# Performance work log

Hardware: AMD Instinct MI355X
Metric: run time of the kernel (lower is better)

## Reference

```python
import jax, jax.numpy as jnp
import numpy as np

B, L, D, H = 2, 2048, 1024, 16
HD = D // H
HID = 4 * D
EPS = 1e-5


def setup_inputs() -> dict:
    key = jax.random.key(0)
    ks = jax.random.split(key, 16)
    s = 0.02
    inp = {
        "x": jax.random.normal(ks[0], (B, L, D), jnp.float32),
        "mask": jnp.triu(jnp.ones((L, L), bool), k=1),  # True above diagonal -> masked
        "wq": jax.random.normal(ks[1], (D, D), jnp.float32) * s,
        "wk": jax.random.normal(ks[2], (D, D), jnp.float32) * s,
        "wv": jax.random.normal(ks[3], (D, D), jnp.float32) * s,
        "wo": jax.random.normal(ks[4], (D, D), jnp.float32) * s,
        "ln1_g": jnp.ones((D,), jnp.float32),
        "ln1_b": jnp.zeros((D,), jnp.float32),
        "ln2_g": jnp.ones((D,), jnp.float32),
        "ln2_b": jnp.zeros((D,), jnp.float32),
        "w1": jax.random.normal(ks[5], (HID, D), jnp.float32) * s,
        "b1": jnp.zeros((HID,), jnp.float32),
        "wg": jax.random.normal(ks[6], (HID, D), jnp.float32) * s,
        "w2": jax.random.normal(ks[7], (D, HID), jnp.float32) * s,
        "b2": jnp.zeros((D,), jnp.float32),
    }
    return inp


def _layernorm(x, g, b):
    mu = jnp.mean(x, axis=-1, keepdims=True)
    var = jnp.mean(jnp.square(x - mu), axis=-1, keepdims=True)
    return (x - mu) * jax.lax.rsqrt(var + EPS) * g + b


def _attention(h, mask, wq, wk, wv, wo):
    b, l, d = h.shape
    scale = HD ** -0.5
    # torch Linear: y = x @ W.T (W is [out, in])
    q = (h @ wq.T).reshape(b, l, H, HD)
    k = (h @ wk.T).reshape(b, l, H, HD)
    v = (h @ wv.T).reshape(b, l, H, HD)
    attn = jnp.einsum("bqhd,bkhd->bhqk", q, k) * scale
    attn = jnp.where(mask[None, None, :, :], -jnp.inf, attn)
    pos_bias = jnp.arange(l, dtype=attn.dtype) * 0.01  # additive bias along key axis
    attn = attn + pos_bias[None, None, None, :]
    attn = jax.nn.softmax(attn, axis=-1)
    out = jnp.einsum("bhqk,bkhd->bqhd", attn, v).reshape(b, l, d)
    return out @ wo.T


def _ffn(h, w1, b1, wg, w2, b2):
    return (jax.nn.silu(h @ w1.T + b1) * (h @ wg.T)) @ w2.T + b2


def reference(x, mask, wq, wk, wv, wo, ln1_g, ln1_b, ln2_g, ln2_b, w1, b1, wg, w2, b2):
    x = x + _attention(_layernorm(x, ln1_g, ln1_b), mask, wq, wk, wv, wo)
    x = x + _ffn(_layernorm(x, ln2_g, ln2_b), w1, b1, wg, w2, b2)
    return x
```

## Files before the change

### kernel.cpp

```cpp
#include <hip/hip_runtime.h>

#define ML   2048
#define MD   1024
#define MH   16
#define MHD  64
#define MB   2
#define MM   4096
#define MHID 4096

typedef unsigned short u16;
typedef short bf16x8 __attribute__((ext_vector_type(8)));
typedef float f32x4 __attribute__((ext_vector_type(4)));

__device__ __forceinline__ u16 f2bf(float f) {
    union { float f; unsigned u; } c; c.f = f;
    unsigned r = c.u + 0x7fffu + ((c.u >> 16) & 1u);
    return (u16)(r >> 16);
}
__device__ __forceinline__ float bf2f(u16 h) {
    union { unsigned u; float f; } c; c.u = ((unsigned)h) << 16;
    return c.f;
}

__device__ __forceinline__ void async_copy16(const u16* g, u16* l) {
    __builtin_amdgcn_global_load_lds(
        (const __attribute__((address_space(1))) void*)g,
        (__attribute__((address_space(3))) void*)l, 16, 0, 0);
}

struct ConvPack {
    const float* src[13];
    u16* dst[13];
    int n[13];
    int start[14];
};

__global__ __launch_bounds__(256)
void conv_all(ConvPack p)
{
    const int bx = blockIdx.x;
    int seg = 0;
    while (seg < 12 && bx >= p.start[seg + 1]) ++seg;
    const int local = bx - p.start[seg];
    const int idx = (local * 256 + threadIdx.x) * 8;
    if (idx >= p.n[seg]) return;
    const float* in = p.src[seg];
    const float4 a = *(const float4*)(in + idx);
    const float4 b = *(const float4*)(in + idx + 4);
    union { bf16x8 v; u16 s[8]; } u;
    u.s[0] = f2bf(a.x); u.s[1] = f2bf(a.y); u.s[2] = f2bf(a.z); u.s[3] = f2bf(a.w);
    u.s[4] = f2bf(b.x); u.s[5] = f2bf(b.y); u.s[6] = f2bf(b.z); u.s[7] = f2bf(b.w);
    *(bf16x8*)&p.dst[seg][idx] = u.v;
}

template<int MI, int NI>
__device__ __forceinline__ void gemm_core(
    const u16* __restrict__ A, const u16* __restrict__ Bm,
    int m0, int n0, int K, u16* As, u16* Bs, f32x4 (&acc)[MI][NI])
{
    constexpr int TM = MI * 32;
    constexpr int TN = NI * 32;
    const int tid  = threadIdx.x;
    const int wave = tid >> 6, lane = tid & 63;
    const int wm = wave & 1, wn = wave >> 1;
    const int l15 = lane & 15, quad = lane >> 4;

    const int srow = wave * 16 + (lane >> 2);
    const int scol = (lane & 3) * 8;
    const u16* Ag = A  + (size_t)(m0 + srow) * K + scol;
    const u16* Bg = Bm + (size_t)(n0 + srow) * K + scol;
    u16* Asw = As + srow * 32 + scol;
    u16* Bsw = Bs + srow * 32 + scol;

    f32x4 zero4 = {0.f, 0.f, 0.f, 0.f};
#pragma unroll
    for (int mi = 0; mi < MI; ++mi)
#pragma unroll
        for (int ni = 0; ni < NI; ++ni) acc[mi][ni] = zero4;

    for (int k0 = 0; k0 < K; k0 += 32) {
        __syncthreads();
#pragma unroll
        for (int p = 0; p < TM / 64; ++p)
            async_copy16(Ag + k0 + (size_t)p * 64 * K, Asw + p * 64 * 32);
#pragma unroll
        for (int p = 0; p < TN / 64; ++p)
            async_copy16(Bg + k0 + (size_t)p * 64 * K, Bsw + p * 64 * 32);
        __syncthreads();

        bf16x8 af[MI], bfr[NI];
#pragma unroll
        for (int mi = 0; mi < MI; ++mi)
            af[mi] = *(const bf16x8*)&As[(wm * MI * 16 + mi * 16 + l15) * 32 + quad * 8];
#pragma unroll
        for (int ni = 0; ni < NI; ++ni)
            bfr[ni] = *(const bf16x8*)&Bs[(wn * NI * 16 + ni * 16 + l15) * 32 + quad * 8];
#pragma unroll
        for (int mi = 0; mi < MI; ++mi)
#pragma unroll
            for (int ni = 0; ni < NI; ++ni)
                acc[mi][ni] = __builtin_amdgcn_mfma_f32_16x16x32_bf16(
                    af[mi], bfr[ni], acc[mi][ni], 0, 0, 0);
    }
}

__global__ __launch_bounds__(256)
void ln_kernel(const float* __restrict__ xin,
               const u16* __restrict__ g, const u16* __restrict__ bb,
               u16* __restrict__ out)
{
    const int row = blockIdx.x;
    const int tid = threadIdx.x;
    const float4 t = *(const float4*)(xin + (size_t)row * MD + tid * 4);
    float v[4] = {t.x, t.y, t.z, t.w};
    float s  = v[0] + v[1] + v[2] + v[3];
    float s2 = v[0]*v[0] + v[1]*v[1] + v[2]*v[2] + v[3]*v[3];
#pragma unroll
    for (int off = 1; off < 64; off <<= 1) {
        s  += __shfl_xor(s,  off);
        s2 += __shfl_xor(s2, off);
    }
    __shared__ float red[8];
    const int wave = tid >> 6, lane = tid & 63;
    if (lane == 0) { red[wave] = s; red[4 + wave] = s2; }
    __syncthreads();
    s  = red[0] + red[1] + red[2] + red[3];
    s2 = red[4] + red[5] + red[6] + red[7];
    const float mu  = s * (1.0f / MD);
    const float var = fmaxf(s2 * (1.0f / MD) - mu * mu, 0.0f);
    const float rs  = rsqrtf(var + 1e-5f);
    const ushort4 gv = *(const ushort4*)&g[tid * 4];
    const ushort4 bv = *(const ushort4*)&bb[tid * 4];
    ushort4 o;
    o.x = f2bf((v[0] - mu) * rs * bf2f(gv.x) + bf2f(bv.x));
    o.y = f2bf((v[1] - mu) * rs * bf2f(gv.y) + bf2f(bv.y));
    o.z = f2bf((v[2] - mu) * rs * bf2f(gv.z) + bf2f(bv.z));
    o.w = f2bf((v[3] - mu) * rs * bf2f(gv.w) + bf2f(bv.w));
    *(ushort4*)&out[(size_t)row * MD + tid * 4] = o;
}

__global__ __launch_bounds__(256, 2)
void gemm_qkv(const u16* __restrict__ ln, const u16* __restrict__ wq,
              const u16* __restrict__ wk, const u16* __restrict__ wv,
              u16* __restrict__ q, u16* __restrict__ k, u16* __restrict__ vt)
{
    __shared__ __align__(16) u16 As[128 * 32];
    __shared__ __align__(16) u16 Bs[128 * 32];
    const int z = blockIdx.z;
    const u16* Bm = (z == 0) ? wq : (z == 1) ? wk : wv;
    const int m0 = blockIdx.x * 128, n0 = blockIdx.y * 128;
    f32x4 acc[4][4];
    gemm_core<4, 4>(ln, Bm, m0, n0, MD, As, Bs, acc);

    const int tid = threadIdx.x;
    const int wave = tid >> 6, lane = tid & 63;
    const int wm = wave & 1, wn = wave >> 1, l15 = lane & 15, quad = lane >> 4;
    if (z < 2) {
        u16* out = (z == 0) ? q : k;
        const float scale = (z == 0) ? 0.125f : 1.0f;
#pragma unroll
        for (int mi = 0; mi < 4; ++mi)
#pragma unroll
            for (int ni = 0; ni < 4; ++ni)
#pragma unroll
                for (int r = 0; r < 4; ++r) {
                    const int row = m0 + wm * 64 + mi * 16 + quad * 4 + r;
                    const int col = n0 + wn * 64 + ni * 16 + l15;
                    out[(size_t)row * MD + col] = f2bf(acc[mi][ni][r] * scale);
                }
    } else {
#pragma unroll
        for (int mi = 0; mi < 4; ++mi)
#pragma unroll
            for (int ni = 0; ni < 4; ++ni) {
                const int row0 = m0 + wm * 64 + mi * 16 + quad * 4;
                const int col  = n0 + wn * 64 + ni * 16 + l15;
                const int bb = row0 >> 11, l = row0 & (ML - 1);
                const int hh = col >> 6,  hd = col & (MHD - 1);
                ushort4 pk;
                pk.x = f2bf(acc[mi][ni][0]);
                pk.y = f2bf(acc[mi][ni][1]);
                pk.z = f2bf(acc[mi][ni][2]);
                pk.w = f2bf(acc[mi][ni][3]);
                *(ushort4*)&vt[((size_t)(bb * MH + hh) * MHD + hd) * ML + l] = pk;
            }
    }
}

__global__ __launch_bounds__(256, 2)
void attn_kernel(const u16* __restrict__ Q, const u16* __restrict__ Kb,
                 const u16* __restrict__ Vt, u16* __restrict__ O)
{
    __shared__ __align__(16) u16 Ks[64 * 64];
    __shared__ __align__(16) u16 Vs[64 * 64];
    __shared__ __align__(16) u16 Pl[4][16 * 72];
    const int tid = threadIdx.x, wave = tid >> 6, lane = tid & 63;
    const int quad = lane >> 4, l15 = lane & 15;
    const int idx = blockIdx.x;
    const int qt = (ML / 64 - 1) - (idx >> 5);
    const int hb = idx & 31;
    const int h = hb & 15, b = hb >> 4;
    const int q0 = qt * 64;
    const int qrow = q0 + wave * 16;
    const float L2E = 1.44269504f;
    const float C1 = 0.01f * L2E;
    const float C2 = -32.0f * L2E;

    u16* Plw = Pl[wave];

    const size_t qoff = ((size_t)(b * ML + qrow + l15)) * MD + h * MHD + quad * 8;
    const bf16x8 aq0 = *(const bf16x8*)&Q[qoff];
    const bf16x8 aq1 = *(const bf16x8*)&Q[qoff + 32];

    const int str = tid >> 3;
    const int sj  = tid & 7;
    const int sjx = (sj ^ (str & 7)) * 8;
    const u16* Kg = Kb + (size_t)(b * ML) * MD + h * MHD;
    const u16* Vg = Vt + (size_t)((b * MH + h) * MHD) * ML;

    const int rsw0 = ((quad    ) ^ (l15 & 7)) * 8;
    const int rsw1 = ((quad + 4) ^ (l15 & 7)) * 8;

    bf16x8 onesf;
    {
        const short v = (l15 == 0) ? (short)0x3F80 : (short)0;
        onesf = (bf16x8){v, v, v, v, v, v, v, v};
    }

    f32x4 zero4 = {0.f, 0.f, 0.f, 0.f};
    f32x4 Oacc[4];
    f32x4 lsum = zero4;
#pragma unroll
    for (int i = 0; i < 4; ++i) Oacc[i] = zero4;

    for (int kt = 0; kt <= qt; ++kt) {
        const int k0 = kt * 64;

        __syncthreads();
        async_copy16(Kg + (size_t)(k0 + str) * MD + sjx,        Ks + tid * 8);
        async_copy16(Kg + (size_t)(k0 + 32 + str) * MD + sjx,   Ks + 2048 + tid * 8);
        async_copy16(Vg + (size_t)str * ML + k0 + sjx,          Vs + tid * 8);
        async_copy16(Vg + (size_t)(32 + str) * ML + k0 + sjx,   Vs + 2048 + tid * 8);
        __syncthreads();

        f32x4 s[4];
#pragma unroll
        for (int jn = 0; jn < 4; ++jn) {
            const int krow = (jn * 16 + l15) * 64;
            const bf16x8 k0f = *(const bf16x8*)&Ks[krow + rsw0];
            const bf16x8 k1f = *(const bf16x8*)&Ks[krow + rsw1];
            f32x4 z = zero4;
            z = __builtin_amdgcn_mfma_f32_16x16x32_bf16(aq0, k0f, z, 0, 0, 0);
            z = __builtin_amdgcn_mfma_f32_16x16x32_bf16(aq1, k1f, z, 0, 0, 0);
            s[jn] = z;
        }

        const bool diag = (kt == qt);
#pragma unroll
        for (int jn = 0; jn < 4; ++jn) {
            const int key = k0 + jn * 16 + l15;
            const float pbm = fmaf((float)key, C1, C2);
#pragma unroll
            for (int r = 0; r < 4; ++r) {
                float val = fmaf(s[jn][r], L2E, pbm);
                if (diag && key > qrow + quad * 4 + r) val = -30000.f;
                union { float f; unsigned u; } c;
                c.f = exp2f(val);
                Plw[(quad * 4 + r) * 72 + jn * 16 + l15] = (u16)(c.u >> 16);
            }
        }

        bf16x8 vv[4][2];
#pragma unroll
        for (int j = 0; j < 4; ++j) {
            const int vrow = (j * 16 + l15) * 64;
            vv[j][0] = *(const bf16x8*)&Vs[vrow + rsw0];
            vv[j][1] = *(const bf16x8*)&Vs[vrow + rsw1];
        }

        const bf16x8 ap0 = *(const bf16x8*)&Plw[l15 * 72 + quad * 8];
        const bf16x8 ap1 = *(const bf16x8*)&Plw[l15 * 72 + 32 + quad * 8];
#pragma unroll
        for (int j = 0; j < 4; ++j) {
            Oacc[j] = __builtin_amdgcn_mfma_f32_16x16x32_bf16(ap0, vv[j][0], Oacc[j], 0, 0, 0);
            Oacc[j] = __builtin_amdgcn_mfma_f32_16x16x32_bf16(ap1, vv[j][1], Oacc[j], 0, 0, 0);
        }
        lsum = __builtin_amdgcn_mfma_f32_16x16x32_bf16(ap0, onesf, lsum, 0, 0, 0);
        lsum = __builtin_amdgcn_mfma_f32_16x16x32_bf16(ap1, onesf, lsum, 0, 0, 0);
    }

#pragma unroll
    for (int r = 0; r < 4; ++r) {
        const float l = __shfl(lsum[r], lane & 48);
        const float inv = 1.0f / l;
        const int row = qrow + quad * 4 + r;
#pragma unroll
        for (int j = 0; j < 4; ++j) {
            const int col = h * MHD + j * 16 + l15;
            O[((size_t)(b * ML + row)) * MD + col] = f2bf(Oacc[j][r] * inv);
        }
    }
}

__global__ __launch_bounds__(256, 2)
void gemm_wo(const u16* __restrict__ ao, const u16* __restrict__ wo,
             const float* __restrict__ x, float* __restrict__ h1)
{
    __shared__ __align__(16) u16 As[128 * 32];
    __shared__ __align__(16) u16 Bs[128 * 32];
    const int m0 = blockIdx.x * 128, n0 = blockIdx.y * 128;
    f32x4 acc[4][4];
    gemm_core<4, 4>(ao, wo, m0, n0, MD, As, Bs, acc);
    const int tid = threadIdx.x;
    const int wave = tid >> 6, lane = tid & 63;
    const int wm = wave & 1, wn = wave >> 1, l15 = lane & 15, quad = lane >> 4;
#pragma unroll
    for (int mi = 0; mi < 4; ++mi)
#pragma unroll
        for (int ni = 0; ni < 4; ++ni)
#pragma unroll
            for (int r = 0; r < 4; ++r) {
                const int row = m0 + wm * 64 + mi * 16 + quad * 4 + r;
                const int col = n0 + wn * 64 + ni * 16 + l15;
                const size_t idx = (size_t)row * MD + col;
                h1[idx] = acc[mi][ni][r] + x[idx];
            }
}

__global__ __launch_bounds__(256, 2)
void gemm_u(const u16* __restrict__ ln, const u16* __restrict__ w1,
            const u16* __restrict__ b1, u16* __restrict__ u)
{
    __shared__ __align__(16) u16 As[128 * 32];
    __shared__ __align__(16) u16 Bs[128 * 32];
    const int m0 = blockIdx.x * 128, n0 = blockIdx.y * 128;
    f32x4 acc[4][4];
    gemm_core<4, 4>(ln, w1, m0, n0, MD, As, Bs, acc);
    const int tid = threadIdx.x;
    const int wave = tid >> 6, lane = tid & 63;
    const int wm = wave & 1, wn = wave >> 1, l15 = lane & 15, quad = lane >> 4;
#pragma unroll
    for (int mi = 0; mi < 4; ++mi)
#pragma unroll
        for (int ni = 0; ni < 4; ++ni)
#pragma unroll
            for (int r = 0; r < 4; ++r) {
                const int row = m0 + wm * 64 + mi * 16 + quad * 4 + r;
                const int col = n0 + wn * 64 + ni * 16 + l15;
                u[(size_t)row * MHID + col] = f2bf(acc[mi][ni][r] + bf2f(b1[col]));
            }
}

__global__ __launch_bounds__(256, 2)
void gemm_g(const u16* __restrict__ ln, const u16* __restrict__ wg,
            const u16* __restrict__ u, u16* __restrict__ hf)
{
    __shared__ __align__(16) u16 As[128 * 32];
    __shared__ __align__(16) u16 Bs[128 * 32];
    const int m0 = blockIdx.x * 128, n0 = blockIdx.y * 128;
    f32x4 acc[4][4];
    gemm_core<4, 4>(ln, wg, m0, n0, MD, As, Bs, acc);
    const int tid = threadIdx.x;
    const int wave = tid >> 6, lane = tid & 63;
    const int wm = wave & 1, wn = wave >> 1, l15 = lane & 15, quad = lane >> 4;
#pragma unroll
    for (int mi = 0; mi < 4; ++mi)
#pragma unroll
        for (int ni = 0; ni < 4; ++ni)
#pragma unroll
            for (int r = 0; r < 4; ++r) {
                const int row = m0 + wm * 64 + mi * 16 + quad * 4 + r;
                const int col = n0 + wn * 64 + ni * 16 + l15;
                const float uv = bf2f(u[(size_t)row * MHID + col]);
                const float si = uv / (1.0f + __expf(-uv));
                hf[(size_t)row * MHID + col] = f2bf(si * acc[mi][ni][r]);
            }
}

__global__ __launch_bounds__(256, 2)
void gemm_w2(const u16* __restrict__ hf, const u16* __restrict__ w2,
             const u16* __restrict__ b2, const float* __restrict__ h1,
             float* __restrict__ out)
{
    __shared__ __align__(16) u16 As[128 * 32];
    __shared__ __align__(16) u16 Bs[128 * 32];
    const int m0 = blockIdx.x * 128, n0 = blockIdx.y * 128;
    f32x4 acc[4][4];
    gemm_core<4, 4>(hf, w2, m0, n0, MHID, As, Bs, acc);
    const int tid = threadIdx.x;
    const int wave = tid >> 6, lane = tid & 63;
    const int wm = wave & 1, wn = wave >> 1, l15 = lane & 15, quad = lane >> 4;
#pragma unroll
    for (int mi = 0; mi < 4; ++mi)
#pragma unroll
        for (int ni = 0; ni < 4; ++ni)
#pragma unroll
            for (int r = 0; r < 4; ++r) {
                const int row = m0 + wm * 64 + mi * 16 + quad * 4 + r;
                const int col = n0 + wn * 64 + ni * 16 + l15;
                const size_t idx = (size_t)row * MD + col;
                out[idx] = acc[mi][ni][r] + bf2f(b2[col]) + h1[idx];
            }
}

extern "C" void kernel_launch(void* const* d_in, const int* in_sizes, int n_in,
                              void* d_out, int out_size, void* d_ws, size_t ws_size,
                              hipStream_t stream)
{
    const float* x    = (const float*)d_in[0];
    const float* wq   = (const float*)d_in[2];
    const float* wk   = (const float*)d_in[3];
    const float* wv   = (const float*)d_in[4];
    const float* wo   = (const float*)d_in[5];
    const float* ln1g = (const float*)d_in[6];
    const float* ln1b = (const float*)d_in[7];
    const float* ln2g = (const float*)d_in[8];
    const float* ln2b = (const float*)d_in[9];
    const float* w1   = (const float*)d_in[10];
    const float* b1   = (const float*)d_in[11];
    const float* wgp  = (const float*)d_in[12];
    const float* w2   = (const float*)d_in[13];
    const float* b2   = (const float*)d_in[14];
    float* out = (float*)d_out;

    char* ws = (char*)d_ws;
    u16*  wqb  = (u16*)(ws);
    u16*  wkb  = (u16*)(ws + ((size_t)2  << 20));
    u16*  wvb  = (u16*)(ws + ((size_t)4  << 20));
    u16*  wob  = (u16*)(ws + ((size_t)6  << 20));
    u16*  w1b  = (u16*)(ws + ((size_t)8  << 20));
    u16*  wgb  = (u16*)(ws + ((size_t)16 << 20));
    u16*  w2b  = (u16*)(ws + ((size_t)24 << 20));
    char* vec  = ws + ((size_t)32 << 20);
    u16*  l1g  = (u16*)(vec);
    u16*  l1b  = (u16*)(vec + 4096);
    u16*  l2g  = (u16*)(vec + 8192);
    u16*  l2b  = (u16*)(vec + 12288);
    u16*  b1b  = (u16*)(vec + 16384);
    u16*  b2b  = (u16*)(vec + 24576);
    u16*   ln  = (u16*)(ws + ((size_t)33 << 20));
    u16*   q   = (u16*)(ws + ((size_t)41 << 20));
    u16*   k   = (u16*)(ws + ((size_t)49 << 20));
    u16*   vt  = (u16*)(ws + ((size_t)57 << 20));
    u16*   ao  = ln;
    float* h1  = (float*)(ws + ((size_t)41 << 20));
    u16*   u   = (u16*)(ws + ((size_t)57 << 20));
    u16*   hf  = (u16*)(ws + ((size_t)89 << 20));

    const int NW = MD * MD;
    const int NF = MHID * MD;
    ConvPack cp;
    const float* srcs[13] = {wq, wk, wv, wo, w1, wgp, w2, ln1g, ln1b, ln2g, ln2b, b1, b2};
    u16* dsts[13]         = {wqb, wkb, wvb, wob, w1b, wgb, w2b, l1g, l1b, l2g, l2b, b1b, b2b};
    int  ns[13]           = {NW, NW, NW, NW, NF, NF, NF, MD, MD, MD, MD, MHID, MD};
    int start = 0;
    for (int i = 0; i < 13; ++i) {
        cp.src[i] = srcs[i]; cp.dst[i] = dsts[i]; cp.n[i] = ns[i];
        cp.start[i] = start;
        start += (ns[i] + 2047) / 2048;
    }
    cp.start[13] = start;
    conv_all<<<start, 256, 0, stream>>>(cp);

    ln_kernel<<<MM, 256, 0, stream>>>(x, l1g, l1b, ln);
    gemm_qkv<<<dim3(MM / 128, MD / 128, 3), 256, 0, stream>>>(ln, wqb, wkb, wvb, q, k, vt);
    attn_kernel<<<(ML / 64) * MH * MB, 256, 0, stream>>>(q, k, vt, ao);
    gemm_wo<<<dim3(MM / 128, MD / 128), 256, 0, stream>>>(ao, wob, x, h1);
    ln_kernel<<<MM, 256, 0, stream>>>(h1, l2g, l2b, ln);
    gemm_u<<<dim3(MM / 128, MHID / 128), 256, 0, stream>>>(ln, w1b, b1b, u);
    gemm_g<<<dim3(MM / 128, MHID / 128), 256, 0, stream>>>(ln, wgb, u, hf);
    gemm_w2<<<dim3(MM / 128, MD / 128), 256, 0, stream>>>(hf, w2b, b2b, h1, out);
}
```

Baseline: 423.0 us.

## Fuse FFN up/gate GEMMs, split-K down projection with atomics, smaller Wo tiles

Merges the separate up and gate GEMMs into one kernel that shares the A tile and computes SiLU-gating in the epilogue, removing the intermediate u buffer round-trip. The second layernorm now also initializes the output with residual plus b2. The W2 GEMM is then split over K into two halves that accumulate into the output with float atomics, doubling the grid. The Wo GEMM uses 64-row tiles to launch more blocks. In exchange, the fused kernel holds more accumulator registers and more LDS, the atomics make summation order nondeterministic, and the output is read-modify-written.

```diff
diff --git a/kernel.cpp b/kernel.cpp
--- a/kernel.cpp
+++ b/kernel.cpp
@@ -56,7 +56,8 @@
 template<int MI, int NI>
 __device__ __forceinline__ void gemm_core(
     const u16* __restrict__ A, const u16* __restrict__ Bm,
-    int m0, int n0, int K, u16* As, u16* Bs, f32x4 (&acc)[MI][NI])
+    int m0, int n0, int lda, int ldb, int K,
+    u16* As, u16* Bs, f32x4 (&acc)[MI][NI])
 {
     constexpr int TM = MI * 32;
     constexpr int TN = NI * 32;
@@ -67,8 +68,8 @@
 
     const int srow = wave * 16 + (lane >> 2);
     const int scol = (lane & 3) * 8;
-    const u16* Ag = A  + (size_t)(m0 + srow) * K + scol;
-    const u16* Bg = Bm + (size_t)(n0 + srow) * K + scol;
+    const u16* Ag = A  + (size_t)(m0 + srow) * lda + scol;
+    const u16* Bg = Bm + (size_t)(n0 + srow) * ldb + scol;
     u16* Asw = As + srow * 32 + scol;
     u16* Bsw = Bs + srow * 32 + scol;
 
@@ -82,10 +83,10 @@
         __syncthreads();
 #pragma unroll
         for (int p = 0; p < TM / 64; ++p)
-            async_copy16(Ag + k0 + (size_t)p * 64 * K, Asw + p * 64 * 32);
+            async_copy16(Ag + k0 + (size_t)p * 64 * lda, Asw + p * 64 * 32);
 #pragma unroll
         for (int p = 0; p < TN / 64; ++p)
-            async_copy16(Bg + k0 + (size_t)p * 64 * K, Bsw + p * 64 * 32);
+            async_copy16(Bg + k0 + (size_t)p * 64 * ldb, Bsw + p * 64 * 32);
         __syncthreads();
 
         bf16x8 af[MI], bfr[NI];
@@ -107,12 +108,22 @@
 __global__ __launch_bounds__(256)
 void ln_kernel(const float* __restrict__ xin,
                const u16* __restrict__ g, const u16* __restrict__ bb,
-               u16* __restrict__ out)
+               u16* __restrict__ out,
+               const u16* __restrict__ rbias, float* __restrict__ oinit)
 {
     const int row = blockIdx.x;
     const int tid = threadIdx.x;
     const float4 t = *(const float4*)(xin + (size_t)row * MD + tid * 4);
     float v[4] = {t.x, t.y, t.z, t.w};
+    if (oinit) {
+        const ushort4 rb = *(const ushort4*)&rbias[tid * 4];
+        float4 oi;
+        oi.x = v[0] + bf2f(rb.x);
+        oi.y = v[1] + bf2f(rb.y);
+        oi.z = v[2] + bf2f(rb.z);
+        oi.w = v[3] + bf2f(rb.w);
+        *(float4*)&oinit[(size_t)row * MD + tid * 4] = oi;
+    }
     float s  = v[0] + v[1] + v[2] + v[3];
     float s2 = v[0]*v[0] + v[1]*v[1] + v[2]*v[2] + v[3]*v[3];
 #pragma unroll
@@ -150,7 +161,7 @@
     const u16* Bm = (z == 0) ? wq : (z == 1) ? wk : wv;
     const int m0 = blockIdx.x * 128, n0 = blockIdx.y * 128;
     f32x4 acc[4][4];
-    gemm_core<4, 4>(ln, Bm, m0, n0, MD, As, Bs, acc);
+    gemm_core<4, 4>(ln, Bm, m0, n0, MD, MD, MD, As, Bs, acc);
 
     const int tid = threadIdx.x;
     const int wave = tid >> 6, lane = tid & 63;
@@ -306,21 +317,21 @@
 void gemm_wo(const u16* __restrict__ ao, const u16* __restrict__ wo,
              const float* __restrict__ x, float* __restrict__ h1)
 {
-    __shared__ __align__(16) u16 As[128 * 32];
+    __shared__ __align__(16) u16 As[64 * 32];
     __shared__ __align__(16) u16 Bs[128 * 32];
-    const int m0 = blockIdx.x * 128, n0 = blockIdx.y * 128;
-    f32x4 acc[4][4];
-    gemm_core<4, 4>(ao, wo, m0, n0, MD, As, Bs, acc);
+    const int m0 = blockIdx.x * 64, n0 = blockIdx.y * 128;
+    f32x4 acc[2][4];
+    gemm_core<2, 4>(ao, wo, m0, n0, MD, MD, MD, As, Bs, acc);
     const int tid = threadIdx.x;
     const int wave = tid >> 6, lane = tid & 63;
     const int wm = wave & 1, wn = wave >> 1, l15 = lane & 15, quad = lane >> 4;
 #pragma unroll
-    for (int mi = 0; mi < 4; ++mi)
+    for (int mi = 0; mi < 2; ++mi)
 #pragma unroll
         for (int ni = 0; ni < 4; ++ni)
 #pragma unroll
             for (int r = 0; r < 4; ++r) {
-                const int row = m0 + wm * 64 + mi * 16 + quad * 4 + r;
+                const int row = m0 + wm * 32 + mi * 16 + quad * 4 + r;
                 const int col = n0 + wn * 64 + ni * 16 + l15;
                 const size_t idx = (size_t)row * MD + col;
                 h1[idx] = acc[mi][ni][r] + x[idx];
@@ -328,14 +339,89 @@
 }
 
 __global__ __launch_bounds__(256, 2)
-void gemm_u(const u16* __restrict__ ln, const u16* __restrict__ w1,
-            const u16* __restrict__ b1, u16* __restrict__ u)
+void gemm_ug(const u16* __restrict__ ln, const u16* __restrict__ w1,
+             const u16* __restrict__ wg, const u16* __restrict__ b1,
+             u16* __restrict__ hf)
+{
+    __shared__ __align__(16) u16 As[128 * 32];
+    __shared__ __align__(16) u16 B1s[128 * 32];
+    __shared__ __align__(16) u16 B2s[128 * 32];
+    const int m0 = blockIdx.x * 128, n0 = blockIdx.y * 128;
+    const int tid = threadIdx.x;
+    const int wave = tid >> 6, lane = tid & 63;
+    const int wm = wave & 1, wn = wave >> 1;
+    const int l15 = lane & 15, quad = lane >> 4;
+
+    const int srow = wave * 16 + (lane >> 2);
+    const int scol = (lane & 3) * 8;
+    const u16* Ag  = ln + (size_t)(m0 + srow) * MD + scol;
+    const u16* B1g = w1 + (size_t)(n0 + srow) * MD + scol;
+    const u16* B2g = wg + (size_t)(n0 + srow) * MD + scol;
+    u16* Asw  = As  + srow * 32 + scol;
+    u16* B1sw = B1s + srow * 32 + scol;
+    u16* B2sw = B2s + srow * 32 + scol;
+
+    f32x4 zero4 = {0.f, 0.f, 0.f, 0.f};
+    f32x4 au[4][4], ag[4][4];
+#pragma unroll
+    for (int mi = 0; mi < 4; ++mi)
+#pragma unroll
+        for (int ni = 0; ni < 4; ++ni) { au[mi][ni] = zero4; ag[mi][ni] = zero4; }
+
+    for (int k0 = 0; k0 < MD; k0 += 32) {
+        __syncthreads();
+#pragma unroll
+        for (int p = 0; p < 2; ++p) {
+            async_copy16(Ag  + k0 + (size_t)p * 64 * MD, Asw  + p * 64 * 32);
+            async_copy16(B1g + k0 + (size_t)p * 64 * MD, B1sw + p * 64 * 32);
+            async_copy16(B2g + k0 + (size_t)p * 64 * MD, B2sw + p * 64 * 32);
+        }
+        __syncthreads();
+
+        bf16x8 af[4], f1[4], f2[4];
+#pragma unroll
+        for (int mi = 0; mi < 4; ++mi)
+            af[mi] = *(const bf16x8*)&As[(wm * 64 + mi * 16 + l15) * 32 + quad * 8];
+#pragma unroll
+        for (int ni = 0; ni < 4; ++ni) {
+            f1[ni] = *(const bf16x8*)&B1s[(wn * 64 + ni * 16 + l15) * 32 + quad * 8];
+            f2[ni] = *(const bf16x8*)&B2s[(wn * 64 + ni * 16 + l15) * 32 + quad * 8];
+        }
+#pragma unroll
+        for (int mi = 0; mi < 4; ++mi)
+#pragma unroll
+            for (int ni = 0; ni < 4; ++ni) {
+                au[mi][ni] = __builtin_amdgcn_mfma_f32_16x16x32_bf16(
+                    af[mi], f1[ni], au[mi][ni], 0, 0, 0);
+                ag[mi][ni] = __builtin_amdgcn_mfma_f32_16x16x32_bf16(
+                    af[mi], f2[ni], ag[mi][ni], 0, 0, 0);
+            }
+    }
+
+#pragma unroll
+    for (int mi = 0; mi < 4; ++mi)
+#pragma unroll
+        for (int ni = 0; ni < 4; ++ni)
+#pragma unroll
+            for (int r = 0; r < 4; ++r) {
+                const int row = m0 + wm * 64 + mi * 16 + quad * 4 + r;
+                const int col = n0 + wn * 64 + ni * 16 + l15;
+                const float uv = au[mi][ni][r] + bf2f(b1[col]);
+                const float si = uv / (1.0f + __expf(-uv));
+                hf[(size_t)row * MHID + col] = f2bf(si * ag[mi][ni][r]);
+            }
+}
+
+__global__ __launch_bounds__(256, 2)
+void gemm_w2(const u16* __restrict__ hf, const u16* __restrict__ w2,
+             float* __restrict__ out)
 {
     __shared__ __align__(16) u16 As[128 * 32];
     __shared__ __align__(16) u16 Bs[128 * 32];
     const int m0 = blockIdx.x * 128, n0 = blockIdx.y * 128;
+    const int kz = blockIdx.z * 2048;
     f32x4 acc[4][4];
-    gemm_core<4, 4>(ln, w1, m0, n0, MD, As, Bs, acc);
+    gemm_core<4, 4>(hf + kz, w2 + kz, m0, n0, MHID, MHID, 2048, As, Bs, acc);
     const int tid = threadIdx.x;
     const int wave = tid >> 6, lane = tid & 63;
     const int wm = wave & 1, wn = wave >> 1, l15 = lane & 15, quad = lane >> 4;
@@ -347,59 +433,7 @@
             for (int r = 0; r < 4; ++r) {
                 const int row = m0 + wm * 64 + mi * 16 + quad * 4 + r;
                 const int col = n0 + wn * 64 + ni * 16 + l15;
-                u[(size_t)row * MHID + col] = f2bf(acc[mi][ni][r] + bf2f(b1[col]));
-            }
-}
-
-__global__ __launch_bounds__(256, 2)
-void gemm_g(const u16* __restrict__ ln, const u16* __restrict__ wg,
-            const u16* __restrict__ u, u16* __restrict__ hf)
-{
-    __shared__ __align__(16) u16 As[128 * 32];
-    __shared__ __align__(16) u16 Bs[128 * 32];
-    const int m0 = blockIdx.x * 128, n0 = blockIdx.y * 128;
-    f32x4 acc[4][4];
-    gemm_core<4, 4>(ln, wg, m0, n0, MD, As, Bs, acc);
-    const int tid = threadIdx.x;
-    const int wave = tid >> 6, lane = tid & 63;
-    const int wm = wave & 1, wn = wave >> 1, l15 = lane & 15, quad = lane >> 4;
-#pragma unroll
-    for (int mi = 0; mi < 4; ++mi)
-#pragma unroll
-        for (int ni = 0; ni < 4; ++ni)
-#pragma unroll
-            for (int r = 0; r < 4; ++r) {
-                const int row = m0 + wm * 64 + mi * 16 + quad * 4 + r;
-                const int col = n0 + wn * 64 + ni * 16 + l15;
-                const float uv = bf2f(u[(size_t)row * MHID + col]);
-                const float si = uv / (1.0f + __expf(-uv));
-                hf[(size_t)row * MHID + col] = f2bf(si * acc[mi][ni][r]);
-            }
-}
-
-__global__ __launch_bounds__(256, 2)
-void gemm_w2(const u16* __restrict__ hf, const u16* __restrict__ w2,
-             const u16* __restrict__ b2, const float* __restrict__ h1,
-             float* __restrict__ out)
-{
-    __shared__ __align__(16) u16 As[128 * 32];
-    __shared__ __align__(16) u16 Bs[128 * 32];
-    const int m0 = blockIdx.x * 128, n0 = blockIdx.y * 128;
-    f32x4 acc[4][4];
-    gemm_core<4, 4>(hf, w2, m0, n0, MHID, As, Bs, acc);
-    const int tid = threadIdx.x;
-    const int wave = tid >> 6, lane = tid & 63;
-    const int wm = wave & 1, wn = wave >> 1, l15 = lane & 15, quad = lane >> 4;
-#pragma unroll
-    for (int mi = 0; mi < 4; ++mi)
-#pragma unroll
-        for (int ni = 0; ni < 4; ++ni)
-#pragma unroll
-            for (int r = 0; r < 4; ++r) {
-                const int row = m0 + wm * 64 + mi * 16 + quad * 4 + r;
-                const int col = n0 + wn * 64 + ni * 16 + l15;
-                const size_t idx = (size_t)row * MD + col;
-                out[idx] = acc[mi][ni][r] + bf2f(b2[col]) + h1[idx];
+                unsafeAtomicAdd(&out[(size_t)row * MD + col], acc[mi][ni][r]);
             }
 }
 
@@ -444,7 +478,6 @@
     u16*   vt  = (u16*)(ws + ((size_t)57 << 20));
     u16*   ao  = ln;
     float* h1  = (float*)(ws + ((size_t)41 << 20));
-    u16*   u   = (u16*)(ws + ((size_t)57 << 20));
     u16*   hf  = (u16*)(ws + ((size_t)89 << 20));
 
     const int NW = MD * MD;
@@ -462,12 +495,11 @@
     cp.start[13] = start;
     conv_all<<<start, 256, 0, stream>>>(cp);
 
-    ln_kernel<<<MM, 256, 0, stream>>>(x, l1g, l1b, ln);
+    ln_kernel<<<MM, 256, 0, stream>>>(x, l1g, l1b, ln, nullptr, nullptr);
     gemm_qkv<<<dim3(MM / 128, MD / 128, 3), 256, 0, stream>>>(ln, wqb, wkb, wvb, q, k, vt);
     attn_kernel<<<(ML / 64) * MH * MB, 256, 0, stream>>>(q, k, vt, ao);
-    gemm_wo<<<dim3(MM / 128, MD / 128), 256, 0, stream>>>(ao, wob, x, h1);
-    ln_kernel<<<MM, 256, 0, stream>>>(h1, l2g, l2b, ln);
-    gemm_u<<<dim3(MM / 128, MHID / 128), 256, 0, stream>>>(ln, w1b, b1b, u);
-    gemm_g<<<dim3(MM / 128, MHID / 128), 256, 0, stream>>>(ln, wgb, u, hf);
-    gemm_w2<<<dim3(MM / 128, MD / 128), 256, 0, stream>>>(hf, w2b, b2b, h1, out);
-}
+    gemm_wo<<<dim3(MM / 64, MD / 128), 256, 0, stream>>>(ao, wob, x, h1);
+    ln_kernel<<<MM, 256, 0, stream>>>(h1, l2g, l2b, ln, b2b, out);
+    gemm_ug<<<dim3(MM / 128, MHID / 128), 256, 0, stream>>>(ln, w1b, wgb, b1b, hf);
+    gemm_w2<<<dim3(MM / 128, MD / 128, 2), 256, 0, stream>>>(hf, w2b, out);
+}
```

Result: faster. 398.0 us (-5.9%).
